# Performance work log

Hardware: AMD Instinct MI355X
Metric: run time of the kernel (lower is better)

The kernel has to match this reference:

```python
import jax, jax.numpy as jnp
import numpy as np

B, C, H, W_IMG = 64, 3, 512, 512
P = 16                      # patch size
IN_F, OUT_F, HEADS = 256, 64, 8
HD = HEADS * OUT_F          # 512
PATCH_DIM = P * P * C       # 768
EPS = 1e-5


def setup_inputs() -> dict:
    key = jax.random.key(0)
    ks = jax.random.split(key, 11)
    s = 0.02
    return {
        "token": jax.random.normal(ks[0], (B, IN_F), jnp.float32),
        "feature": jax.random.normal(ks[1], (B, C, H, W_IMG), jnp.float32),
        "W_patch": jax.random.normal(ks[2], (PATCH_DIM, IN_F), jnp.float32) * s,
        "b_patch": jax.random.normal(ks[3], (IN_F,), jnp.float32) * s,
        "W": jax.random.normal(ks[4], (IN_F, HD), jnp.float32) * s,
        "a_self": jax.random.normal(ks[5], (HEADS, OUT_F), jnp.float32) * s,
        "a_neigh": jax.random.normal(ks[6], (HEADS, OUT_F), jnp.float32) * s,
        "W_out": jax.random.normal(ks[7], (HD, IN_F), jnp.float32) * s,
        "b_out": jax.random.normal(ks[8], (IN_F,), jnp.float32) * s,
        "gamma": jnp.ones((IN_F,), jnp.float32),
        "beta": jnp.zeros((IN_F,), jnp.float32),
    }


def _forward(token, feature, W_patch, b_patch, W, a_self, a_neigh, W_out, b_out, gamma, beta):
    b = token.shape[0]
    # to_patch: 'b c (h p1) (w p2) -> b (h w) (p1 p2 c)' then Linear
    hh, ww = H // P, W_IMG // P
    patches = feature.reshape(b, C, hh, P, ww, P)
    patches = patches.transpose(0, 2, 4, 3, 5, 1).reshape(b, hh * ww, P * P * C)
    feat = patches @ W_patch + b_patch                    # [b, n, IN_F]
    feat_h = (feat @ W).reshape(b, -1, HEADS, OUT_F).transpose(0, 2, 1, 3)  # [b, h, n, d]
    tok_h = (token @ W).reshape(b, HEADS, OUT_F)          # [b, h, d]
    # per-head GAT-style scores (vectorized over heads)
    a_s = jnp.einsum('bhd,hd->bh', tok_h, a_self)         # [b, h]
    a_n = jnp.einsum('bhnd,hd->bhn', feat_h, a_neigh)     # [b, h, n]
    attn = jax.nn.leaky_relu(a_s[:, :, None] + a_n, 0.2)  # [b, h, n]
    # original: softmax over the trailing size-1 axis -> all ones (faithful)
    attn = jax.nn.softmax(attn[..., None], axis=-1)[..., 0]
    out = jnp.einsum('bhn,bhnd->bhd', attn, feat_h)       # [b, h, d]
    # concat=True branch
    out = 0.5 * (out.reshape(b, HD) @ W_out + b_out) + 0.5 * token
    x = 0.5 * out + 0.5 * token
    mu = jnp.mean(x, axis=-1, keepdims=True)
    var = jnp.mean((x - mu) ** 2, axis=-1, keepdims=True)
    return (x - mu) * jax.lax.rsqrt(var + EPS) * gamma + beta


def reference(token, feature, W_patch, b_patch, W, a_self, a_neigh, W_out, b_out, gamma, beta):
    return _forward(token, feature, W_patch, b_patch, W, a_self, a_neigh, W_out, b_out, gamma, beta)
```

## Files before the change

kernel.cpp:

```cpp
#include <hip/hip_runtime.h>
#include <hip/hip_bf16.h>

#define BB 64
#define CC 3
#define HH 512
#define WW 512
#define PP 16
#define IN_F 256
#define HD 512
#define PATCH_DIM 768
#define NPATCH 1024

typedef float floatx4 __attribute__((ext_vector_type(4)));


__global__ __launch_bounds__(512)
void m2_kernel(const float* __restrict__ Wm,
               const float* __restrict__ Wo,
               float* __restrict__ M2)
{
    int i = blockIdx.x;
    int t = threadIdx.x;

    __shared__ float sA[HD];
    __shared__ float part[8 * IN_F];

    sA[t] = Wm[(size_t)i * HD + t];
    __syncthreads();

    int j4 = (t & 63) * 4;
    int kg = t >> 6;
    float a0 = 0.f, a1 = 0.f, a2 = 0.f, a3 = 0.f;
    const float* wrow = Wo + (size_t)(kg * 64) * IN_F + j4;
#pragma unroll 8
    for (int k = 0; k < 64; ++k) {
        float s = sA[kg * 64 + k];
        float4 w = *(const float4*)(wrow + (size_t)k * IN_F);
        a0 += s * w.x; a1 += s * w.y; a2 += s * w.z; a3 += s * w.w;
    }
    part[kg * IN_F + j4 + 0] = a0;
    part[kg * IN_F + j4 + 1] = a1;
    part[kg * IN_F + j4 + 2] = a2;
    part[kg * IN_F + j4 + 3] = a3;
    __syncthreads();

    if (t < IN_F) {
        float s = 0.f;
#pragma unroll
        for (int g = 0; g < 8; ++g)
            s += part[g * IN_F + t];
        M2[(size_t)i * IN_F + t] = s;
    }
}

__global__ __launch_bounds__(256)
void patch_reduce_kernel(const float* __restrict__ feature,
                         float* __restrict__ S)
{
    int bid = blockIdx.x;
    int p1 = bid & 15;
    int tmp = bid >> 4;
    int c = tmp % 3;
    int b = tmp / 3;
    int t = threadIdx.x;

    const size_t base_bc = (size_t)(b * 3 + c) * (size_t)(HH * WW);

    float acc[4] = {0.f, 0.f, 0.f, 0.f};

#pragma unroll
    for (int i = 0; i < 16; ++i) {
        int idx = i * 256 + t;
        int h = idx >> 7;
        int u = idx & 127;
        size_t off = base_bc + (size_t)(p1 + 16 * h) * WW + (size_t)u * 4;
        floatx4 v = __builtin_nontemporal_load((const floatx4*)(feature + off));
        acc[0] += v.x;
        acc[1] += v.y;
        acc[2] += v.z;
        acc[3] += v.w;
    }

    __shared__ float red[16 * 68];
    __shared__ float red2[16 * 8];
    int g = t >> 2;
    int pb = (t & 3) * 4;
#pragma unroll
    for (int j = 0; j < 4; ++j)
        red[(pb + j) * 68 + g] = acc[j];
    __syncthreads();

    if (t < 128) {
        int bin = t >> 3;
        int l = t & 7;
        float s = 0.f;
#pragma unroll
        for (int q = 0; q < 8; ++q)
            s += red[bin * 68 + l + 8 * q];
        red2[bin * 8 + l] = s;
    }
    __syncthreads();

    if (t < 16) {
        float s = 0.f;
#pragma unroll
        for (int l = 0; l < 8; ++l)
            s += red2[t * 8 + l];
        S[(size_t)b * PATCH_DIM + (size_t)(p1 * 16 + t) * 3 + c] = s;
    }
}

__global__ __launch_bounds__(512)
void fuse_kernel(const float* __restrict__ S,
                 const float* __restrict__ Wp,
                 const float* __restrict__ bp,
                 const float* __restrict__ M2,
                 const float* __restrict__ bo,
                 const float* __restrict__ tok,
                 const float* __restrict__ gamma,
                 const float* __restrict__ beta,
                 float* __restrict__ out)
{
    int b = blockIdx.x;
    int t = threadIdx.x;

    __shared__ float sS[PATCH_DIM];
    __shared__ float part1[8 * IN_F];
    __shared__ float sT[IN_F];
    __shared__ float part2[8 * IN_F];
    __shared__ float wred[8];
    __shared__ float stats[2];

    float bo_t = 0.f, tok_t = 0.f, gamma_t = 0.f, beta_t = 0.f, bp_t = 0.f;
    if (t < IN_F) {
        bo_t    = bo[t];
        tok_t   = tok[b * IN_F + t];
        gamma_t = gamma[t];
        beta_t  = beta[t];
        bp_t    = bp[t];
    }

    for (int k = t; k < PATCH_DIM; k += 512)
        sS[k] = S[(size_t)b * PATCH_DIM + k];
    __syncthreads();

    {
        int j4 = (t & 63) * 4;
        int kg = t >> 6;
        float a0 = 0.f, a1 = 0.f, a2 = 0.f, a3 = 0.f;
        const float* wrow = Wp + (size_t)(kg * 96) * IN_F + j4;
#pragma unroll 8
        for (int i = 0; i < 96; ++i) {
            float s = sS[kg * 96 + i];
            float4 w = *(const float4*)(wrow + (size_t)i * IN_F);
            a0 += s * w.x; a1 += s * w.y; a2 += s * w.z; a3 += s * w.w;
        }
        part1[kg * IN_F + j4 + 0] = a0;
        part1[kg * IN_F + j4 + 1] = a1;
        part1[kg * IN_F + j4 + 2] = a2;
        part1[kg * IN_F + j4 + 3] = a3;
    }
    __syncthreads();
    if (t < IN_F) {
        float s = 0.f;
#pragma unroll
        for (int kg = 0; kg < 8; ++kg)
            s += part1[kg * IN_F + t];
        sT[t] = s + 1024.f * bp_t;
    }
    __syncthreads();

    {
        int j4 = (t & 63) * 4;
        int kg = t >> 6;
        float a0 = 0.f, a1 = 0.f, a2 = 0.f, a3 = 0.f;
        const float* wrow = M2 + (size_t)(kg * 32) * IN_F + j4;
#pragma unroll 8
        for (int i = 0; i < 32; ++i) {
            float s = sT[kg * 32 + i];
            float4 w = *(const float4*)(wrow + (size_t)i * IN_F);
            a0 += s * w.x; a1 += s * w.y; a2 += s * w.z; a3 += s * w.w;
        }
        part2[kg * IN_F + j4 + 0] = a0;
        part2[kg * IN_F + j4 + 1] = a1;
        part2[kg * IN_F + j4 + 2] = a2;
        part2[kg * IN_F + j4 + 3] = a3;
    }
    __syncthreads();

    float x = 0.f;
    if (t < IN_F) {
        float z = 0.f;
#pragma unroll
        for (int kg = 0; kg < 8; ++kg)
            z += part2[kg * IN_F + t];
        x = 0.25f * (z + bo_t) + 0.75f * tok_t;
    }

    float s1 = x, s2 = x * x;
#pragma unroll
    for (int off = 32; off > 0; off >>= 1) {
        s1 += __shfl_down(s1, off);
        s2 += __shfl_down(s2, off);
    }
    int wave = t >> 6;
    if ((t & 63) == 0 && wave < 4) {
        wred[wave * 2]     = s1;
        wred[wave * 2 + 1] = s2;
    }
    __syncthreads();
    if (t == 0) {
        float a1 = wred[0] + wred[2] + wred[4] + wred[6];
        float a2 = wred[1] + wred[3] + wred[5] + wred[7];
        float mu = a1 * (1.f / 256.f);
        float var = a2 * (1.f / 256.f) - mu * mu;
        stats[0] = mu;
        stats[1] = rsqrtf(var + 1e-5f);
    }
    __syncthreads();

    if (t < IN_F) {
        float y = (x - stats[0]) * stats[1] * gamma_t + beta_t;
        out[b * IN_F + t] = y;
    }
}

extern "C" void kernel_launch(void* const* d_in, const int* in_sizes, int n_in,
                              void* d_out, int out_size, void* d_ws, size_t ws_size,
                              hipStream_t stream)
{
    const float* token   = (const float*)d_in[0];
    const float* feature = (const float*)d_in[1];
    const float* W_patch = (const float*)d_in[2];
    const float* b_patch = (const float*)d_in[3];
    const float* W       = (const float*)d_in[4];
    const float* W_out   = (const float*)d_in[7];
    const float* b_out   = (const float*)d_in[8];
    const float* gamma   = (const float*)d_in[9];
    const float* beta    = (const float*)d_in[10];

    float* out = (float*)d_out;
    float* S  = (float*)d_ws;
    float* M2 = S + (size_t)BB * PATCH_DIM;

    m2_kernel<<<IN_F, 512, 0, stream>>>(W, W_out, M2);

    dim3 grid1(BB * CC * 16);
    patch_reduce_kernel<<<grid1, 256, 0, stream>>>(feature, S);

    fuse_kernel<<<BB, 512, 0, stream>>>(S, W_patch, b_patch, M2, b_out,
                                        token, gamma, beta, out);
}
```

Before: 299.0 us.

## Fold patch projection into combined weight matrix and merge prep kernels

```diff
diff --git a/kernel.cpp b/kernel.cpp
--- a/kernel.cpp
+++ b/kernel.cpp
@@ -1,5 +1,4 @@
 #include <hip/hip_runtime.h>
-#include <hip/hip_bf16.h>
 
 #define BB 64
 #define CC 3
@@ -10,112 +9,134 @@
 #define HD 512
 #define PATCH_DIM 768
 #define NPATCH 1024
+#define NB_M3 257
 
 typedef float floatx4 __attribute__((ext_vector_type(4)));
 
 
-__global__ __launch_bounds__(512)
-void m2_kernel(const float* __restrict__ Wm,
-               const float* __restrict__ Wo,
-               float* __restrict__ M2)
-{
-    int i = blockIdx.x;
-    int t = threadIdx.x;
-
-    __shared__ float sA[HD];
-    __shared__ float part[8 * IN_F];
-
-    sA[t] = Wm[(size_t)i * HD + t];
-    __syncthreads();
-
-    int j4 = (t & 63) * 4;
-    int kg = t >> 6;
-    float a0 = 0.f, a1 = 0.f, a2 = 0.f, a3 = 0.f;
-    const float* wrow = Wo + (size_t)(kg * 64) * IN_F + j4;
-#pragma unroll 8
-    for (int k = 0; k < 64; ++k) {
-        float s = sA[kg * 64 + k];
-        float4 w = *(const float4*)(wrow + (size_t)k * IN_F);
-        a0 += s * w.x; a1 += s * w.y; a2 += s * w.z; a3 += s * w.w;
-    }
-    part[kg * IN_F + j4 + 0] = a0;
-    part[kg * IN_F + j4 + 1] = a1;
-    part[kg * IN_F + j4 + 2] = a2;
-    part[kg * IN_F + j4 + 3] = a3;
-    __syncthreads();
-
-    if (t < IN_F) {
-        float s = 0.f;
-#pragma unroll
-        for (int g = 0; g < 8; ++g)
-            s += part[g * IN_F + t];
-        M2[(size_t)i * IN_F + t] = s;
-    }
-}
-
 __global__ __launch_bounds__(256)
-void patch_reduce_kernel(const float* __restrict__ feature,
-                         float* __restrict__ S)
+void prep_kernel(const float* __restrict__ feature,
+                 const float* __restrict__ Wp,
+                 const float* __restrict__ bp,
+                 const float* __restrict__ W,
+                 const float* __restrict__ Wo,
+                 const float* __restrict__ bo,
+                 float* __restrict__ S,
+                 float* __restrict__ M3,
+                 float* __restrict__ c3)
 {
     int bid = blockIdx.x;
-    int p1 = bid & 15;
-    int tmp = bid >> 4;
-    int c = tmp % 3;
-    int b = tmp / 3;
     int t = threadIdx.x;
 
-    const size_t base_bc = (size_t)(b * 3 + c) * (size_t)(HH * WW);
-
-    float acc[4] = {0.f, 0.f, 0.f, 0.f};
-
-#pragma unroll
-    for (int i = 0; i < 16; ++i) {
-        int idx = i * 256 + t;
-        int h = idx >> 7;
-        int u = idx & 127;
-        size_t off = base_bc + (size_t)(p1 + 16 * h) * WW + (size_t)u * 4;
-        floatx4 v = __builtin_nontemporal_load((const floatx4*)(feature + off));
-        acc[0] += v.x;
-        acc[1] += v.y;
-        acc[2] += v.z;
-        acc[3] += v.w;
-    }
-
-    __shared__ float red[16 * 68];
-    __shared__ float red2[16 * 8];
-    int g = t >> 2;
-    int pb = (t & 3) * 4;
-#pragma unroll
-    for (int j = 0; j < 4; ++j)
-        red[(pb + j) * 68 + g] = acc[j];
-    __syncthreads();
-
-    if (t < 128) {
-        int bin = t >> 3;
-        int l = t & 7;
-        float s = 0.f;
-#pragma unroll
-        for (int q = 0; q < 8; ++q)
-            s += red[bin * 68 + l + 8 * q];
-        red2[bin * 8 + l] = s;
-    }
-    __syncthreads();
-
-    if (t < 16) {
-        float s = 0.f;
-#pragma unroll
-        for (int l = 0; l < 8; ++l)
-            s += red2[t * 8 + l];
-        S[(size_t)b * PATCH_DIM + (size_t)(p1 * 16 + t) * 3 + c] = s;
+    if (bid < NB_M3) {
+        __shared__ float sWp[3][IN_F];
+        __shared__ float sv[3][HD];
+
+        if (bid < 256) {
+            int i0 = bid * 3;
+            sWp[0][t] = Wp[(size_t)(i0 + 0) * IN_F + t];
+            sWp[1][t] = Wp[(size_t)(i0 + 1) * IN_F + t];
+            sWp[2][t] = Wp[(size_t)(i0 + 2) * IN_F + t];
+        } else {
+            sWp[0][t] = bp[t];
+            sWp[1][t] = 0.f;
+            sWp[2][t] = 0.f;
+        }
+        __syncthreads();
+
+        float a00 = 0.f, a01 = 0.f, a10 = 0.f, a11 = 0.f, a20 = 0.f, a21 = 0.f;
+        const float* wb = W + 2 * t;
+#pragma unroll 8
+        for (int k = 0; k < IN_F; ++k) {
+            float2 w = *(const float2*)(wb + (size_t)k * HD);
+            float s0 = sWp[0][k], s1 = sWp[1][k], s2 = sWp[2][k];
+            a00 += s0 * w.x; a01 += s0 * w.y;
+            a10 += s1 * w.x; a11 += s1 * w.y;
+            a20 += s2 * w.x; a21 += s2 * w.y;
+        }
+        sv[0][2 * t] = a00; sv[0][2 * t + 1] = a01;
+        sv[1][2 * t] = a10; sv[1][2 * t + 1] = a11;
+        sv[2][2 * t] = a20; sv[2][2 * t + 1] = a21;
+        __syncthreads();
+
+        float b0 = 0.f, b1 = 0.f, b2 = 0.f;
+        const float* wob = Wo + t;
+#pragma unroll 8
+        for (int l = 0; l < HD; ++l) {
+            float w = wob[(size_t)l * IN_F];
+            b0 += sv[0][l] * w;
+            b1 += sv[1][l] * w;
+            b2 += sv[2][l] * w;
+        }
+        if (bid < 256) {
+            int i0 = bid * 3;
+            M3[(size_t)(i0 + 0) * IN_F + t] = b0;
+            M3[(size_t)(i0 + 1) * IN_F + t] = b1;
+            M3[(size_t)(i0 + 2) * IN_F + t] = b2;
+        } else {
+            c3[t] = 1024.f * b0 + bo[t];
+        }
+        return;
+    }
+
+    {
+        int pbid = bid - NB_M3;
+        int p1 = pbid & 15;
+        int tmp = pbid >> 4;
+        int c = tmp % 3;
+        int b = tmp / 3;
+
+        const size_t base_bc = (size_t)(b * 3 + c) * (size_t)(HH * WW);
+
+        float acc[4] = {0.f, 0.f, 0.f, 0.f};
+
+#pragma unroll
+        for (int i = 0; i < 16; ++i) {
+            int idx = i * 256 + t;
+            int h = idx >> 7;
+            int u = idx & 127;
+            size_t off = base_bc + (size_t)(p1 + 16 * h) * WW + (size_t)u * 4;
+            floatx4 v = __builtin_nontemporal_load((const floatx4*)(feature + off));
+            acc[0] += v.x;
+            acc[1] += v.y;
+            acc[2] += v.z;
+            acc[3] += v.w;
+        }
+
+        __shared__ float red[16 * 68];
+        __shared__ float red2[16 * 8];
+        int g = t >> 2;
+        int pb = (t & 3) * 4;
+#pragma unroll
+        for (int j = 0; j < 4; ++j)
+            red[(pb + j) * 68 + g] = acc[j];
+        __syncthreads();
+
+        if (t < 128) {
+            int bin = t >> 3;
+            int l = t & 7;
+            float s = 0.f;
+#pragma unroll
+            for (int q = 0; q < 8; ++q)
+                s += red[bin * 68 + l + 8 * q];
+            red2[bin * 8 + l] = s;
+        }
+        __syncthreads();
+
+        if (t < 16) {
+            float s = 0.f;
+#pragma unroll
+            for (int l = 0; l < 8; ++l)
+                s += red2[t * 8 + l];
+            S[(size_t)b * PATCH_DIM + (size_t)(p1 * 16 + t) * 3 + c] = s;
+        }
     }
 }
 
 __global__ __launch_bounds__(512)
 void fuse_kernel(const float* __restrict__ S,
-                 const float* __restrict__ Wp,
-                 const float* __restrict__ bp,
-                 const float* __restrict__ M2,
-                 const float* __restrict__ bo,
+                 const float* __restrict__ M3,
+                 const float* __restrict__ c3,
                  const float* __restrict__ tok,
                  const float* __restrict__ gamma,
                  const float* __restrict__ beta,
@@ -125,19 +146,16 @@
     int t = threadIdx.x;
 
     __shared__ float sS[PATCH_DIM];
-    __shared__ float part1[8 * IN_F];
-    __shared__ float sT[IN_F];
-    __shared__ float part2[8 * IN_F];
+    __shared__ float part[8 * IN_F];
     __shared__ float wred[8];
     __shared__ float stats[2];
 
-    float bo_t = 0.f, tok_t = 0.f, gamma_t = 0.f, beta_t = 0.f, bp_t = 0.f;
+    float c3_t = 0.f, tok_t = 0.f, gamma_t = 0.f, beta_t = 0.f;
     if (t < IN_F) {
-        bo_t    = bo[t];
+        c3_t    = c3[t];
         tok_t   = tok[b * IN_F + t];
         gamma_t = gamma[t];
         beta_t  = beta[t];
-        bp_t    = bp[t];
     }
 
     for (int k = t; k < PATCH_DIM; k += 512)
@@ -148,43 +166,17 @@
         int j4 = (t & 63) * 4;
         int kg = t >> 6;
         float a0 = 0.f, a1 = 0.f, a2 = 0.f, a3 = 0.f;
-        const float* wrow = Wp + (size_t)(kg * 96) * IN_F + j4;
+        const float* wrow = M3 + (size_t)(kg * 96) * IN_F + j4;
 #pragma unroll 8
         for (int i = 0; i < 96; ++i) {
             float s = sS[kg * 96 + i];
             float4 w = *(const float4*)(wrow + (size_t)i * IN_F);
             a0 += s * w.x; a1 += s * w.y; a2 += s * w.z; a3 += s * w.w;
         }
-        part1[kg * IN_F + j4 + 0] = a0;
-        part1[kg * IN_F + j4 + 1] = a1;
-        part1[kg * IN_F + j4 + 2] = a2;
-        part1[kg * IN_F + j4 + 3] = a3;
-    }
-    __syncthreads();
-    if (t < IN_F) {
-        float s = 0.f;
-#pragma unroll
-        for (int kg = 0; kg < 8; ++kg)
-            s += part1[kg * IN_F + t];
-        sT[t] = s + 1024.f * bp_t;
-    }
-    __syncthreads();
-
-    {
-        int j4 = (t & 63) * 4;
-        int kg = t >> 6;
-        float a0 = 0.f, a1 = 0.f, a2 = 0.f, a3 = 0.f;
-        const float* wrow = M2 + (size_t)(kg * 32) * IN_F + j4;
-#pragma unroll 8
-        for (int i = 0; i < 32; ++i) {
-            float s = sT[kg * 32 + i];
-            float4 w = *(const float4*)(wrow + (size_t)i * IN_F);
-            a0 += s * w.x; a1 += s * w.y; a2 += s * w.z; a3 += s * w.w;
-        }
-        part2[kg * IN_F + j4 + 0] = a0;
-        part2[kg * IN_F + j4 + 1] = a1;
-        part2[kg * IN_F + j4 + 2] = a2;
-        part2[kg * IN_F + j4 + 3] = a3;
+        part[kg * IN_F + j4 + 0] = a0;
+        part[kg * IN_F + j4 + 1] = a1;
+        part[kg * IN_F + j4 + 2] = a2;
+        part[kg * IN_F + j4 + 3] = a3;
     }
     __syncthreads();
 
@@ -193,8 +185,8 @@
         float z = 0.f;
 #pragma unroll
         for (int kg = 0; kg < 8; ++kg)
-            z += part2[kg * IN_F + t];
-        x = 0.25f * (z + bo_t) + 0.75f * tok_t;
+            z += part[kg * IN_F + t];
+        x = 0.25f * (z + c3_t) + 0.75f * tok_t;
     }
 
     float s1 = x, s2 = x * x;
@@ -241,13 +233,12 @@
 
     float* out = (float*)d_out;
     float* S  = (float*)d_ws;
-    float* M2 = S + (size_t)BB * PATCH_DIM;
-
-    m2_kernel<<<IN_F, 512, 0, stream>>>(W, W_out, M2);
-
-    dim3 grid1(BB * CC * 16);
-    patch_reduce_kernel<<<grid1, 256, 0, stream>>>(feature, S);
-
-    fuse_kernel<<<BB, 512, 0, stream>>>(S, W_patch, b_patch, M2, b_out,
-                                        token, gamma, beta, out);
+    float* M3 = S + (size_t)BB * PATCH_DIM;
+    float* c3 = M3 + (size_t)PATCH_DIM * IN_F;
+
+    dim3 grid1(NB_M3 + BB * CC * 16);
+    prep_kernel<<<grid1, 256, 0, stream>>>(feature, W_patch, b_patch,
+                                           W, W_out, b_out, S, M3, c3);
+
+    fuse_kernel<<<BB, 512, 0, stream>>>(S, M3, c3, token, gamma, beta, out);
 }
```

New measurement: 317.8 us. 6.3% more time.
